# Optimization experiments

Measured on AMD Instinct MI355X. Metric: run time of the kernel, lower is better.

Reference implementation:

```python
import jax, jax.numpy as jnp
import numpy as np

K = 4
KS = 7
SHIFT = KS // 2

def setup_inputs() -> dict:
    key = jax.random.key(0)
    ks = jax.random.split(key, 5)
    B, C, H, W = 8, 128, 256, 256
    x = jax.random.normal(ks[0], (B, C, H, W), dtype=jnp.float32)
    guidance = jax.random.normal(ks[1], (B, C, H, W), dtype=jnp.float32)
    basis_filters = jax.random.normal(ks[2], (K, C, KS, KS), dtype=jnp.float32)
    w1 = jax.random.normal(ks[3], (C // 4, C), dtype=jnp.float32) * (1.0 / np.sqrt(C))
    b1 = jnp.zeros((C // 4,), dtype=jnp.float32)
    w2 = jax.random.normal(ks[4], (K, C // 4), dtype=jnp.float32) * (1.0 / np.sqrt(C // 4))
    b2 = jnp.zeros((K,), dtype=jnp.float32)
    return {"x": x, "guidance": guidance, "basis_filters": basis_filters,
            "w1": w1, "b1": b1, "w2": w2, "b2": b2}

def reference(x, guidance, basis_filters, w1, b1, w2, b2):
    B, C, H, W = x.shape
    # guidance vector: global average pool -> MLP -> softmax over k bases
    g = jnp.mean(guidance, axis=(2, 3))                      # [B, C]
    h1 = jax.nn.relu(g @ w1.T + b1)                          # [B, C//4]
    weights = jax.nn.softmax(h1 @ w2.T + b2, axis=1)         # [B, K]
    # dynamic per-sample depthwise kernel: weighted sum of bases
    dyn = jnp.einsum('bk,kcij->bcij', weights, basis_filters)  # [B, C, KS, KS]
    # pad kernel to full (H, W) at the bottom/right, then roll to center at origin
    padded = jnp.pad(dyn, ((0, 0), (0, 0), (0, H - KS), (0, W - KS)))
    centered = jnp.roll(padded, shift=(-SHIFT, -SHIFT), axis=(-2, -1))
    # circular depthwise convolution via FFT
    filt_fft = jnp.fft.rfft2(centered, s=(H, W), axes=(-2, -1))
    x_fft = jnp.fft.rfft2(x, s=(H, W), axes=(-2, -1))
    out = jnp.fft.irfft2(x_fft * filt_fft, s=(H, W), axes=(-2, -1))
    return out
```

## Files before the change

### kernel.cpp

```cpp
#include <hip/hip_runtime.h>

#define HW 256
#define HWMASK 255
#define CH 128
#define BATCH 8
#define NK 4
#define TSY 16
#define NQROW 66
#define NROWS 22
#define NSTAGE (NROWS * NQROW)
#define NT 8

typedef float f32x4 __attribute__((ext_vector_type(4)));

__device__ __forceinline__ void load_lds16(const void* g, void* l) {
    __builtin_amdgcn_global_load_lds((const __attribute__((address_space(1))) void*)g,
                                     (__attribute__((address_space(3))) void*)l, 16, 0, 0);
}

__device__ __forceinline__ void stage_tile(const float* xp, float4* buf, int ystart, int tid) {
    #pragma unroll
    for (int k = 0; k < 6; ++k) {
        int e = (k < 5) ? k * 256 + tid : (NSTAGE - 256) + tid;
        int r = e / NQROW, q = e - r * NQROW;
        int gy = (ystart + r) & HWMASK;
        int gx = (4 * q - 4) & HWMASK;
        load_lds16(xp + gy * HW + gx, &buf[e]);
    }
}

__global__ __launch_bounds__(256) void mean1_kernel(const float* __restrict__ guid,
                                                    float* __restrict__ partial) {
    int blk = blockIdx.x;
    const float4* p = (const float4*)(guid + (size_t)blk * 16384);
    float s = 0.f;
    for (int i = threadIdx.x; i < 4096; i += 256) {
        float4 v = p[i];
        s += (v.x + v.y) + (v.z + v.w);
    }
    for (int off = 32; off; off >>= 1) s += __shfl_down(s, off, 64);
    __shared__ float red[4];
    if ((threadIdx.x & 63) == 0) red[threadIdx.x >> 6] = s;
    __syncthreads();
    if (threadIdx.x == 0) partial[blk] = (red[0] + red[1]) + (red[2] + red[3]);
}

__global__ __launch_bounds__(256) void mlp_kernel(const float* __restrict__ partial,
                                                  const float* __restrict__ w1,
                                                  const float* __restrict__ b1,
                                                  const float* __restrict__ w2,
                                                  const float* __restrict__ b2,
                                                  float* __restrict__ wt) {
    __shared__ float gs[BATCH * CH];
    __shared__ float h1[BATCH * 32];
    __shared__ float lg[BATCH * NK];
    int t = threadIdx.x;
    for (int i = t; i < BATCH * CH; i += 256) {
        float4 v = *(const float4*)(partial + i * 4);
        gs[i] = ((v.x + v.y) + (v.z + v.w)) * (1.0f / 65536.0f);
    }
    __syncthreads();
    {
        int b = t >> 5, j = t & 31;
        float acc = b1[j];
        #pragma unroll 4
        for (int c = 0; c < CH; ++c) acc += gs[b * CH + c] * w1[j * CH + c];
        h1[b * 32 + j] = fmaxf(acc, 0.f);
    }
    __syncthreads();
    if (t < BATCH * NK) {
        int b = t >> 2, k = t & 3;
        float acc = b2[k];
        #pragma unroll
        for (int j = 0; j < 32; ++j) acc += h1[b * 32 + j] * w2[k * 32 + j];
        lg[b * NK + k] = acc;
    }
    __syncthreads();
    if (t < BATCH) {
        int b = t;
        float m = lg[b * 4];
        for (int k = 1; k < 4; ++k) m = fmaxf(m, lg[b * 4 + k]);
        float e[4], s = 0.f;
        for (int k = 0; k < 4; ++k) { e[k] = expf(lg[b * 4 + k] - m); s += e[k]; }
        float inv = 1.0f / s;
        for (int k = 0; k < 4; ++k) wt[b * 4 + k] = e[k] * inv;
    }
}

__global__ __launch_bounds__(256) void dyn_kernel(const float* __restrict__ wt,
                                                  const float* __restrict__ basis,
                                                  float* __restrict__ dynF) {
    int idx = blockIdx.x * 256 + threadIdx.x;
    if (idx >= BATCH * CH * 49) return;
    int ij = idx % 49;
    int bc = idx / 49;
    int c = bc % CH;
    int b = bc / CH;
    float acc = 0.f;
    #pragma unroll
    for (int k = 0; k < NK; ++k)
        acc += wt[b * NK + k] * basis[(k * CH + c) * 49 + ij];
    dynF[bc * 49 + (48 - ij)] = acc;
}

__global__ __launch_bounds__(256) void conv_kernel(const float* __restrict__ x,
                                                   const float* __restrict__ dynF,
                                                   float* __restrict__ out) {
    int bc = blockIdx.x;
    int ybase = blockIdx.y * (NT * TSY);
    __shared__ float4 lds4[3][NSTAGE];
    const float* xp = x + (size_t)bc * (HW * HW);
    float* op = out + (size_t)bc * (HW * HW);
    int tid = threadIdx.x;

    const float* df = dynF + bc * 49;
    float d[49];
    #pragma unroll
    for (int i = 0; i < 49; ++i) d[i] = df[i];

    stage_tile(xp, lds4[0], ybase - 3, tid);
    stage_tile(xp, lds4[1], ybase + TSY - 3, tid);
    asm volatile("s_waitcnt vmcnt(6)" ::: "memory");
    __builtin_amdgcn_s_barrier();

    int tx = tid & 63, ty = tid >> 6;
    int ly0 = 4 * ty;
    int cur = 0, pre = 2;

    #pragma unroll 1
    for (int t = 0; t < NT; ++t) {
        if (t + 2 < NT)
            stage_tile(xp, lds4[pre], ybase + (t + 2) * TSY - 3, tid);

        int y0 = ybase + t * TSY;
        const float4* LB = lds4[cur];
        float acc[4][4] = {};
        #pragma unroll
        for (int rr = 0; rr < 10; ++rr) {
            const float4* rp = &LB[(ly0 + rr) * NQROW + tx];
            float4 A = rp[0], B = rp[1], C = rp[2];
            float v[12] = {A.x, A.y, A.z, A.w, B.x, B.y, B.z, B.w, C.x, C.y, C.z, C.w};
            #pragma unroll
            for (int rq = 0; rq < 4; ++rq) {
                int ii = rr - rq;
                if (ii >= 0 && ii <= 6) {
                    #pragma unroll
                    for (int q = 0; q < 4; ++q) {
                        #pragma unroll
                        for (int jj = 0; jj < 7; ++jj)
                            acc[rq][q] += d[ii * 7 + jj] * v[q + jj + 1];
                    }
                }
            }
        }
        #pragma unroll
        for (int rq = 0; rq < 4; ++rq) {
            f32x4 o = {acc[rq][0], acc[rq][1], acc[rq][2], acc[rq][3]};
            __builtin_nontemporal_store(o, (f32x4*)(op + (y0 + ly0 + rq) * HW + 4 * tx));
        }

        if (t < NT - 1) {
            if (t + 2 < NT) asm volatile("s_waitcnt vmcnt(10)" ::: "memory");
            else            asm volatile("s_waitcnt vmcnt(8)"  ::: "memory");
            __builtin_amdgcn_s_barrier();
        }
        cur = (cur == 2) ? 0 : cur + 1;
        pre = (pre == 2) ? 0 : pre + 1;
    }
}

extern "C" void kernel_launch(void* const* d_in, const int* in_sizes, int n_in,
                              void* d_out, int out_size, void* d_ws, size_t ws_size,
                              hipStream_t stream) {
    const float* x        = (const float*)d_in[0];
    const float* guidance = (const float*)d_in[1];
    const float* basis    = (const float*)d_in[2];
    const float* w1       = (const float*)d_in[3];
    const float* b1       = (const float*)d_in[4];
    const float* w2       = (const float*)d_in[5];
    const float* b2       = (const float*)d_in[6];
    float* out = (float*)d_out;
    float* ws  = (float*)d_ws;

    float* partial = ws;
    float* wt      = ws + 4096;
    float* dynF    = ws + 4096 + 32;

    mean1_kernel<<<4096, 256, 0, stream>>>(guidance, partial);
    mlp_kernel<<<1, 256, 0, stream>>>(partial, w1, b1, w2, b2, wt);
    dyn_kernel<<<(BATCH * CH * 49 + 255) / 256, 256, 0, stream>>>(wt, basis, dynF);
    conv_kernel<<<dim3(BATCH * CH, HW / (NT * TSY)), 256, 0, stream>>>(x, dynF, out);
}
```

Before: 203.8 us.

## Replace async global-to-LDS triple buffering with register-prefetch double buffering

The conv kernel no longer uses global_load_lds direct-to-LDS copies with a three-deep ring. It now prefetches the next tile into six float4 registers per thread, computes the current tile, then writes the registers to the other LDS buffer before a barrier. This cuts LDS use from three stage buffers to two, which may raise occupancy, but it reduces prefetch depth to one tile and adds register pressure plus explicit LDS writes.

```diff
diff --git a/kernel.cpp b/kernel.cpp
--- a/kernel.cpp
+++ b/kernel.cpp
@@ -12,22 +12,6 @@
 #define NT 8
 
 typedef float f32x4 __attribute__((ext_vector_type(4)));
-
-__device__ __forceinline__ void load_lds16(const void* g, void* l) {
-    __builtin_amdgcn_global_load_lds((const __attribute__((address_space(1))) void*)g,
-                                     (__attribute__((address_space(3))) void*)l, 16, 0, 0);
-}
-
-__device__ __forceinline__ void stage_tile(const float* xp, float4* buf, int ystart, int tid) {
-    #pragma unroll
-    for (int k = 0; k < 6; ++k) {
-        int e = (k < 5) ? k * 256 + tid : (NSTAGE - 256) + tid;
-        int r = e / NQROW, q = e - r * NQROW;
-        int gy = (ystart + r) & HWMASK;
-        int gx = (4 * q - 4) & HWMASK;
-        load_lds16(xp + gy * HW + gx, &buf[e]);
-    }
-}
 
 __global__ __launch_bounds__(256) void mean1_kernel(const float* __restrict__ guid,
                                                     float* __restrict__ partial) {
@@ -108,7 +92,7 @@
                                                    float* __restrict__ out) {
     int bc = blockIdx.x;
     int ybase = blockIdx.y * (NT * TSY);
-    __shared__ float4 lds4[3][NSTAGE];
+    __shared__ float4 lds4[2][NSTAGE];
     const float* xp = x + (size_t)bc * (HW * HW);
     float* op = out + (size_t)bc * (HW * HW);
     int tid = threadIdx.x;
@@ -118,22 +102,40 @@
     #pragma unroll
     for (int i = 0; i < 49; ++i) d[i] = df[i];
 
-    stage_tile(xp, lds4[0], ybase - 3, tid);
-    stage_tile(xp, lds4[1], ybase + TSY - 3, tid);
-    asm volatile("s_waitcnt vmcnt(6)" ::: "memory");
-    __builtin_amdgcn_s_barrier();
+    int e0[6], rr0[6], gxq[6];
+    #pragma unroll
+    for (int k = 0; k < 6; ++k) {
+        int e = (k < 5) ? k * 256 + tid : (NSTAGE - 256) + tid;
+        int r = e / NQROW, q = e - r * NQROW;
+        e0[k] = e; rr0[k] = r; gxq[k] = (4 * q - 4) & HWMASK;
+    }
+
+    float4 pf0, pf1, pf2, pf3, pf4, pf5;
+    #define LOADS(ys)                                                            \
+        { int gy;                                                                \
+          gy = ((ys) + rr0[0]) & HWMASK; pf0 = *(const float4*)(xp + gy * HW + gxq[0]); \
+          gy = ((ys) + rr0[1]) & HWMASK; pf1 = *(const float4*)(xp + gy * HW + gxq[1]); \
+          gy = ((ys) + rr0[2]) & HWMASK; pf2 = *(const float4*)(xp + gy * HW + gxq[2]); \
+          gy = ((ys) + rr0[3]) & HWMASK; pf3 = *(const float4*)(xp + gy * HW + gxq[3]); \
+          gy = ((ys) + rr0[4]) & HWMASK; pf4 = *(const float4*)(xp + gy * HW + gxq[4]); \
+          gy = ((ys) + rr0[5]) & HWMASK; pf5 = *(const float4*)(xp + gy * HW + gxq[5]); }
+    #define WRITES(buf)                                                          \
+        { (buf)[e0[0]] = pf0; (buf)[e0[1]] = pf1; (buf)[e0[2]] = pf2;            \
+          (buf)[e0[3]] = pf3; (buf)[e0[4]] = pf4; (buf)[e0[5]] = pf5; }
+
+    LOADS(ybase - 3);
+    WRITES(lds4[0]);
+    __syncthreads();
 
     int tx = tid & 63, ty = tid >> 6;
     int ly0 = 4 * ty;
-    int cur = 0, pre = 2;
 
     #pragma unroll 1
     for (int t = 0; t < NT; ++t) {
-        if (t + 2 < NT)
-            stage_tile(xp, lds4[pre], ybase + (t + 2) * TSY - 3, tid);
+        if (t + 1 < NT) LOADS(ybase + (t + 1) * TSY - 3);
 
         int y0 = ybase + t * TSY;
-        const float4* LB = lds4[cur];
+        const float4* LB = lds4[t & 1];
         float acc[4][4] = {};
         #pragma unroll
         for (int rr = 0; rr < 10; ++rr) {
@@ -159,14 +161,14 @@
             __builtin_nontemporal_store(o, (f32x4*)(op + (y0 + ly0 + rq) * HW + 4 * tx));
         }
 
-        if (t < NT - 1) {
-            if (t + 2 < NT) asm volatile("s_waitcnt vmcnt(10)" ::: "memory");
-            else            asm volatile("s_waitcnt vmcnt(8)"  ::: "memory");
+        if (t + 1 < NT) {
+            WRITES(lds4[(t + 1) & 1]);
+            asm volatile("s_waitcnt lgkmcnt(0)" ::: "memory");
             __builtin_amdgcn_s_barrier();
         }
-        cur = (cur == 2) ? 0 : cur + 1;
-        pre = (pre == 2) ? 0 : pre + 1;
     }
+    #undef LOADS
+    #undef WRITES
 }
 
 extern "C" void kernel_launch(void* const* d_in, const int* in_sizes, int n_in,
```

New measurement: 187.4 us. 8.0% less time.
